# Kernel optimization log

Hardware: AMD Instinct MI355X
Metric: run time of the kernel (lower is better)

## Reference

```python
import jax, jax.numpy as jnp
import numpy as np

N, D, P, NS = 2048, 64, 32, 512  # nnodes, stop_embedding_size, preference_dim, n_active_stops
LEAKY_SLOPE = 0.01
COS_EPS = 1e-8


def setup_inputs() -> dict:
    key = jax.random.key(0)
    ks = jax.random.split(key, 10)
    dist = jax.random.uniform(ks[0], (N, N), dtype=jnp.float32)
    stops = jax.random.randint(ks[1], (NS,), 0, N)
    emb_w = jax.random.normal(ks[2], (N, D), dtype=jnp.float32) * 0.05      # nn.Embedding weight
    lin_l_w = jax.random.normal(ks[3], (P, D), dtype=jnp.float32) * 0.05    # SAGEConv lin_l (aggregated)
    lin_l_b = jnp.zeros((P,), dtype=jnp.float32)
    lin_r_w = jax.random.normal(ks[4], (P, D), dtype=jnp.float32) * 0.05    # SAGEConv lin_r (root)
    edge_w = jax.random.normal(ks[5], (2 * P,), dtype=jnp.float32) * 0.05   # edge_summarizer weight
    edge_b = jnp.zeros((), dtype=jnp.float32)
    in_len = 2 * N + 3 + P
    comb_w = jax.random.normal(ks[6], (N, in_len), dtype=jnp.float32) * 0.02  # combiner weight
    comb_b = jnp.zeros((N,), dtype=jnp.float32)
    return {
        "dist": dist, "emb_w": emb_w,
        "lin_l_w": lin_l_w, "lin_l_b": lin_l_b, "lin_r_w": lin_r_w,
        "edge_w": edge_w, "edge_b": edge_b,
        "comb_w": comb_w, "comb_b": comb_b,
        "stops": stops, "weekday": 3, "vehicles": 5,
    }


def reference(dist, emb_w, lin_l_w, lin_l_b, lin_r_w, edge_w, edge_b,
              comb_w, comb_b, stops, weekday, vehicles):
    dt = emb_w.dtype
    # --- cosine-similarity graph build ---
    norm = jnp.maximum(jnp.linalg.norm(emb_w, axis=1, keepdims=True), COS_EPS)
    xn = emb_w / norm
    sim = xn @ xn.T                                   # [N, N]
    sim = sim * (1.0 - jnp.eye(N, dtype=dt))          # fill_diagonal_(0)
    keep = jnp.zeros((N,), dtype=bool).at[stops].set(True)
    adj = ((sim > 0.5) & keep[:, None] & keep[None, :]).astype(dt)  # [N, N]
    # --- SAGEConv (mean aggregation): lin_l(mean_j x_j) + lin_r(x_i) ---
    deg = jnp.maximum(adj.sum(axis=1, keepdims=True), 1.0)
    agg = (adj @ emb_w) / deg                         # [N, D]
    pref = agg @ lin_l_w.T + lin_l_b + emb_w @ lin_r_w.T   # [N, P]
    # --- all-pairs edge summaries: Linear([pref_i, pref_j]) + LeakyReLU ---
    # equivalent to concat-then-linear, without materializing [N^2, 2P]
    a = pref @ edge_w[:P]                             # [N]
    b = pref @ edge_w[P:]                             # [N]
    es = a[:, None] + b[None, :] + edge_b             # [N, N]
    es = jnp.where(es >= 0, es, LEAKY_SLOPE * es)
    # --- combiner + log-softmax ---
    weekday_feat = jnp.full((N, 1), weekday, dtype=dt)
    vehicle_feat = jnp.full((N, 1), vehicles, dtype=dt)
    stop_feat = keep.astype(dt)[:, None]
    combined = jnp.concatenate([pref, es, dist, weekday_feat, vehicle_feat, stop_feat], axis=1)
    out = combined @ comb_w.T + comb_b                # [N, N]
    return jax.nn.log_softmax(out, axis=1)
```

## Files before the change

### kernel.cpp

```cpp
#include <hip/hip_runtime.h>

typedef unsigned short u16;
typedef __attribute__((ext_vector_type(8))) short bf16x8;
typedef __attribute__((ext_vector_type(4))) float f32x4;

__device__ __forceinline__ u16 f2bf(float f) {
    return (u16)((__float_as_uint(f) + 0x8000u) >> 16);
}

#define N_NODES 2048
#define D_EMB 64
#define P_DIM 32
#define NS_STOPS 512
#define IN_LEN 4131
#define NKT 65

#define SWZ(row, c) ((((row) * 8) + ((c) ^ ((row) & 7))) * 8)

__device__ __forceinline__ void gload16(const u16* g, u16* l) {
    __builtin_amdgcn_global_load_lds((const __attribute__((address_space(1))) void*)g,
                                     (__attribute__((address_space(3))) void*)l, 16, 0, 0);
}

__global__ __launch_bounds__(256) void k_aggpref(const float* __restrict__ emb, const int* __restrict__ stops,
                                                 const float* __restrict__ lin_l_w, const float* __restrict__ lin_l_b,
                                                 const float* __restrict__ lin_r_w, const float* __restrict__ edge_w,
                                                 float* __restrict__ pref, float* __restrict__ av, float* __restrict__ bv,
                                                 float* __restrict__ keepf) {
    __shared__ float se[NS_STOPS][68];
    __shared__ int bm[64];
    __shared__ int kl[NS_STOPS];
    __shared__ float nrm[NS_STOPS];
    __shared__ float xiS[8][D_EMB];
    __shared__ float aggS[8][D_EMB];
    __shared__ float niS[8];
    __shared__ int degS[8];
    __shared__ int kiS[8];
    __shared__ int cnt;
    int t = threadIdx.x;
    int i0 = blockIdx.x * 8;
    if (t < 64) bm[t] = 0;
    if (t == 0) cnt = 0;
    if (t < 8) degS[t] = 0;
    ((float*)aggS)[t] = 0.f;
    ((float*)aggS)[t + 256] = 0.f;
    __syncthreads();
    {
        int s0 = stops[t], s1 = stops[t + 256];
        atomicOr(&bm[s0 >> 5], 1 << (s0 & 31));
        atomicOr(&bm[s1 >> 5], 1 << (s1 & 31));
    }
    __syncthreads();
    {
        int w = bm[t >> 2];
        int base = (t >> 2) * 32 + (t & 3) * 8;
        #pragma unroll
        for (int e = 0; e < 8; ++e)
            if ((w >> ((t & 3) * 8 + e)) & 1) { int p = atomicAdd(&cnt, 1); kl[p] = base + e; }
    }
    if (t < 8) { int i = i0 + t; kiS[t] = (bm[i >> 5] >> (i & 31)) & 1; }
    {
        int n = t >> 5, d = (t & 31) * 2;
        xiS[n][d]     = emb[(i0 + n) * D_EMB + d];
        xiS[n][d + 1] = emb[(i0 + n) * D_EMB + d + 1];
    }
    __syncthreads();
    int nk = cnt;
    for (int u = t >> 3; u < nk; u += 32) {
        int l8 = (t & 7) * 8;
        f32x4 a = *(const f32x4*)&emb[kl[u] * D_EMB + l8];
        f32x4 b = *(const f32x4*)&emb[kl[u] * D_EMB + l8 + 4];
        *(f32x4*)&se[u][l8] = a;
        *(f32x4*)&se[u][l8 + 4] = b;
    }
    if (t < 8) {
        float s = 0.f;
        #pragma unroll
        for (int d = 0; d < D_EMB; ++d) s += xiS[t][d] * xiS[t][d];
        niS[t] = fmaxf(sqrtf(s), 1e-8f);
    }
    __syncthreads();
    for (int u = t; u < nk; u += 256) {
        float s = 0.f;
        #pragma unroll
        for (int d = 0; d < 16; ++d) {
            f32x4 v = *(const f32x4*)&se[u][d * 4];
            s += v[0] * v[0] + v[1] * v[1] + v[2] * v[2] + v[3] * v[3];
        }
        nrm[u] = fmaxf(sqrtf(s), 1e-8f);
    }
    __syncthreads();
    for (int u = t; u < nk; u += 256) {
        int j = kl[u];
        float nj = nrm[u];
        f32x4 er[16];
        #pragma unroll
        for (int d = 0; d < 16; ++d) er[d] = *(const f32x4*)&se[u][d * 4];
        #pragma unroll
        for (int n = 0; n < 8; ++n) {
            if (!kiS[n] || j == i0 + n) continue;
            f32x4 dv = {0.f, 0.f, 0.f, 0.f};
            #pragma unroll
            for (int d = 0; d < 16; ++d) dv += (*(const f32x4*)&xiS[n][d * 4]) * er[d];
            float dot = dv[0] + dv[1] + dv[2] + dv[3];
            if (dot > 0.5f * niS[n] * nj) {
                atomicAdd(&degS[n], 1);
                #pragma unroll
                for (int d = 0; d < 16; ++d) {
                    atomicAdd(&aggS[n][d * 4 + 0], er[d][0]);
                    atomicAdd(&aggS[n][d * 4 + 1], er[d][1]);
                    atomicAdd(&aggS[n][d * 4 + 2], er[d][2]);
                    atomicAdd(&aggS[n][d * 4 + 3], er[d][3]);
                }
            }
        }
    }
    __syncthreads();
    {
        int n = t >> 5, p = t & 31;
        int i = i0 + n;
        float inv = kiS[n] ? (1.f / fmaxf((float)degS[n], 1.0f)) : 0.f;
        float s = lin_l_b[p];
        const float* wl = &lin_l_w[p * D_EMB];
        const float* wr = &lin_r_w[p * D_EMB];
        #pragma unroll
        for (int d = 0; d < D_EMB; ++d) s += aggS[n][d] * inv * wl[d] + xiS[n][d] * wr[d];
        pref[i * P_DIM + p] = s;
        float a = s * edge_w[p];
        float b = s * edge_w[P_DIM + p];
        #pragma unroll
        for (int off = 16; off; off >>= 1) { a += __shfl_xor(a, off, 32); b += __shfl_xor(b, off, 32); }
        if (p == 0) { av[i] = a; bv[i] = b; keepf[i] = (float)kiS[n]; }
    }
}

__global__ __launch_bounds__(256) void k_pack(const float* __restrict__ comb_w, const float* __restrict__ comb_b,
                                              const int* __restrict__ wk_p, const int* __restrict__ vh_p,
                                              const float* __restrict__ dist, const float* __restrict__ pref,
                                              const float* __restrict__ av, const float* __restrict__ bv,
                                              const float* __restrict__ edge_b,
                                              u16* __restrict__ Bp, u16* __restrict__ Ap,
                                              float* __restrict__ cvec, float* __restrict__ w3) {
    int kt = blockIdx.x;
    int ty = blockIdx.y;
    int t = threadIdx.x;
    if (ty < 16) {
        int nt = ty;
        u16* tb = Bp + ((size_t)nt * NKT + kt) * 8192;
        #pragma unroll
        for (int it = 0; it < 4; ++it) {
            int q = t + it * 256;
            int r = q >> 3, c = q & 7;
            int j = nt * 128 + r;
            int k0 = kt * 64 + c * 8;
            const float* cw = comb_w + (size_t)j * IN_LEN;
            bf16x8 v;
            if (k0 < 4096) {
                f32x4 f0, f1;
                __builtin_memcpy(&f0, cw + 32 + k0, 16);
                __builtin_memcpy(&f1, cw + 36 + k0, 16);
                #pragma unroll
                for (int e = 0; e < 4; ++e) { v[e] = (short)f2bf(f0[e]); v[4 + e] = (short)f2bf(f1[e]); }
            } else if (k0 < 4128) {
                f32x4 f0, f1;
                __builtin_memcpy(&f0, cw + (k0 - 4096), 16);
                __builtin_memcpy(&f1, cw + (k0 - 4092), 16);
                #pragma unroll
                for (int e = 0; e < 4; ++e) { v[e] = (short)f2bf(f0[e]); v[4 + e] = (short)f2bf(f1[e]); }
            } else {
                #pragma unroll
                for (int e = 0; e < 8; ++e) v[e] = 0;
            }
            *(bf16x8*)&tb[r * 64 + ((c ^ (r & 7)) * 8)] = v;
        }
        if (kt == 64 && t < 128) {
            int j = nt * 128 + t;
            const float* cw = comb_w + (size_t)j * IN_LEN;
            float wk = (float)wk_p[0], vh = (float)vh_p[0];
            cvec[j] = wk * cw[4128] + vh * cw[4129] + comb_b[j];
            w3[j] = cw[4130];
        }
    } else {
        int rt = ty - 16;
        u16* ta = Ap + ((size_t)rt * NKT + kt) * 4096;
        float eb = edge_b[0];
        #pragma unroll
        for (int it = 0; it < 2; ++it) {
            int q = t + it * 256;
            int r = q >> 3, c = q & 7;
            int row = rt * 64 + r;
            int k0 = kt * 64 + c * 8;
            bf16x8 v;
            if (k0 < 2048) {
                float ab = av[row] + eb;
                f32x4 f0 = *(const f32x4*)(bv + k0);
                f32x4 f1 = *(const f32x4*)(bv + k0 + 4);
                #pragma unroll
                for (int e = 0; e < 4; ++e) {
                    float s0 = ab + f0[e]; s0 = (s0 >= 0.f) ? s0 : 0.01f * s0;
                    float s1 = ab + f1[e]; s1 = (s1 >= 0.f) ? s1 : 0.01f * s1;
                    v[e] = (short)f2bf(s0); v[4 + e] = (short)f2bf(s1);
                }
            } else if (k0 < 4096) {
                const f32x4* dp = (const f32x4*)(dist + (size_t)row * 2048 + (k0 - 2048));
                f32x4 f0 = dp[0], f1 = dp[1];
                #pragma unroll
                for (int e = 0; e < 4; ++e) { v[e] = (short)f2bf(f0[e]); v[4 + e] = (short)f2bf(f1[e]); }
            } else if (k0 < 4128) {
                const f32x4* pp = (const f32x4*)(pref + (size_t)row * P_DIM + (k0 - 4096));
                f32x4 f0 = pp[0], f1 = pp[1];
                #pragma unroll
                for (int e = 0; e < 4; ++e) { v[e] = (short)f2bf(f0[e]); v[4 + e] = (short)f2bf(f1[e]); }
            } else {
                #pragma unroll
                for (int e = 0; e < 8; ++e) v[e] = 0;
            }
            *(bf16x8*)&ta[r * 64 + ((c ^ (r & 7)) * 8)] = v;
        }
    }
}

__global__ __launch_bounds__(256, 4) void k_gemm_d(const u16* __restrict__ Ap, const u16* __restrict__ Bp,
                                                   const float* __restrict__ cvec, const float* __restrict__ w3,
                                                   const float* __restrict__ keepf,
                                                   float* __restrict__ Cout) {
    __shared__ __attribute__((aligned(16))) short As[2][4096];
    __shared__ __attribute__((aligned(16))) short Bs[2][4096];
    int t = threadIdx.x;
    int b = blockIdx.x;
    int c = b & 7, u = b >> 3;
    int mt = (c & 1) * 16 + (u & 15);
    int nt = (c >> 1) * 8 + (u >> 4);
    int tileM = mt * 64, tileN = nt * 64;
    int lane = t & 63;
    int wid = t >> 6;
    int waveM = wid & 1, waveN = wid >> 1;
    int l16 = lane & 15, quad = lane >> 4;

    f32x4 acc[2][2];
    #pragma unroll
    for (int a_ = 0; a_ < 2; ++a_)
        #pragma unroll
        for (int b_ = 0; b_ < 2; ++b_) acc[a_][b_] = (f32x4){0.f, 0.f, 0.f, 0.f};

    const u16* gA = Ap + ((size_t)mt * NKT) * 4096 + t * 8;
    const u16* gB = Bp + ((size_t)(nt >> 1) * NKT) * 8192 + (nt & 1) * 4096 + t * 8;

#define ISSUE(ktv, bb) do { \
        const u16* a0 = gA + (size_t)(ktv) * 4096; \
        const u16* b0 = gB + (size_t)(ktv) * 8192; \
        u16* ad = (u16*)As[bb] + t * 8; \
        u16* bd = (u16*)Bs[bb] + t * 8; \
        gload16(a0, ad); \
        gload16(a0 + 2048, ad + 2048); \
        gload16(b0, bd); \
        gload16(b0 + 2048, bd + 2048); \
    } while (0)

    ISSUE(0, 0);

    int cur = 0;
    for (int kt = 0; kt < NKT; ++kt) {
        __syncthreads();
        if (kt + 1 < NKT) ISSUE(kt + 1, cur ^ 1);
        const short* Asc = As[cur];
        const short* Bsc = Bs[cur];
        #pragma unroll
        for (int kk = 0; kk < 64; kk += 32) {
            int cbase = kk >> 3;
            bf16x8 af[2], bfr[2];
            #pragma unroll
            for (int mi = 0; mi < 2; ++mi) {
                int row = waveM * 32 + mi * 16 + l16;
                af[mi] = *(const bf16x8*)&Asc[SWZ(row, cbase + quad)];
            }
            #pragma unroll
            for (int ni = 0; ni < 2; ++ni) {
                int row = waveN * 32 + ni * 16 + l16;
                bfr[ni] = *(const bf16x8*)&Bsc[SWZ(row, cbase + quad)];
            }
            #pragma unroll
            for (int mi = 0; mi < 2; ++mi)
                #pragma unroll
                for (int ni = 0; ni < 2; ++ni)
                    acc[mi][ni] = __builtin_amdgcn_mfma_f32_16x16x32_bf16(af[mi], bfr[ni], acc[mi][ni], 0, 0, 0);
        }
        cur ^= 1;
    }
#undef ISSUE
    #pragma unroll
    for (int mi = 0; mi < 2; ++mi)
        #pragma unroll
        for (int ni = 0; ni < 2; ++ni) {
            int row0 = tileM + waveM * 32 + mi * 16 + quad * 4;
            int col = tileN + waveN * 32 + ni * 16 + l16;
            float cv = cvec[col], wv = w3[col];
            float* cp = Cout + (size_t)row0 * N_NODES + col;
            #pragma unroll
            for (int rr = 0; rr < 4; ++rr)
                cp[(size_t)rr * N_NODES] = acc[mi][ni][rr] + cv + keepf[row0 + rr] * wv;
        }
}

__global__ __launch_bounds__(256) void k_epi(float* __restrict__ out) {
    int i = blockIdx.x, t = threadIdx.x;
    __shared__ float redmax[4], redsum[4];
    f32x4* orow = (f32x4*)(out + (size_t)i * N_NODES);
    f32x4 v0 = orow[t];
    f32x4 v1 = orow[t + 256];
    float vmax = fmaxf(fmaxf(fmaxf(v0[0], v0[1]), fmaxf(v0[2], v0[3])),
                       fmaxf(fmaxf(v1[0], v1[1]), fmaxf(v1[2], v1[3])));
    #pragma unroll
    for (int off = 32; off; off >>= 1) vmax = fmaxf(vmax, __shfl_xor(vmax, off, 64));
    if ((t & 63) == 0) redmax[t >> 6] = vmax;
    __syncthreads();
    vmax = fmaxf(fmaxf(redmax[0], redmax[1]), fmaxf(redmax[2], redmax[3]));
    float se = 0.f;
    #pragma unroll
    for (int e = 0; e < 4; ++e) se += expf(v0[e] - vmax) + expf(v1[e] - vmax);
    #pragma unroll
    for (int off = 32; off; off >>= 1) se += __shfl_xor(se, off, 64);
    if ((t & 63) == 0) redsum[t >> 6] = se;
    __syncthreads();
    se = redsum[0] + redsum[1] + redsum[2] + redsum[3];
    float lz = vmax + logf(se);
    orow[t] = v0 - lz;
    orow[t + 256] = v1 - lz;
}

extern "C" void kernel_launch(void* const* d_in, const int* in_sizes, int n_in,
                              void* d_out, int out_size, void* d_ws, size_t ws_size,
                              hipStream_t stream) {
    const float* dist    = (const float*)d_in[0];
    const float* emb     = (const float*)d_in[1];
    const float* lin_l_w = (const float*)d_in[2];
    const float* lin_l_b = (const float*)d_in[3];
    const float* lin_r_w = (const float*)d_in[4];
    const float* edge_w  = (const float*)d_in[5];
    const float* edge_b  = (const float*)d_in[6];
    const float* comb_w  = (const float*)d_in[7];
    const float* comb_b  = (const float*)d_in[8];
    const int* stops     = (const int*)d_in[9];
    const int* wk        = (const int*)d_in[10];
    const int* vh        = (const int*)d_in[11];

    char* ws = (char*)d_ws;
    float* pref  = (float*)(ws + 0);
    float* av    = (float*)(ws + 262144);
    float* bv    = (float*)(ws + 270336);
    float* cvec  = (float*)(ws + 278528);
    float* w3    = (float*)(ws + 286720);
    float* keepf = (float*)(ws + 294912);
    u16*   Ap    = (u16*)(ws + 303104);
    u16*   Bp    = (u16*)(ws + 17342464);
    float* out   = (float*)d_out;

    hipLaunchKernelGGL(k_aggpref, dim3(256),    dim3(256), 0, stream, emb, stops,
                       lin_l_w, lin_l_b, lin_r_w, edge_w, pref, av, bv, keepf);
    hipLaunchKernelGGL(k_pack,    dim3(65, 48), dim3(256), 0, stream, comb_w, comb_b, wk, vh,
                       dist, pref, av, bv, edge_b, Bp, Ap, cvec, w3);
    hipLaunchKernelGGL(k_gemm_d,  dim3(1024),   dim3(256), 0, stream, Ap, Bp, cvec, w3, keepf, out);
    hipLaunchKernelGGL(k_epi,     dim3(2048),   dim3(256), 0, stream, out);
}
```

Measured before the change: 188.8 us.

## Load A operand fragments directly from global into registers in MFMA order

```diff
diff --git a/kernel.cpp b/kernel.cpp
--- a/kernel.cpp
+++ b/kernel.cpp
@@ -187,9 +187,9 @@
         #pragma unroll
         for (int it = 0; it < 2; ++it) {
             int q = t + it * 256;
-            int r = q >> 3, c = q & 7;
+            int r = q >> 3, kc = q & 7;
             int row = rt * 64 + r;
-            int k0 = kt * 64 + c * 8;
+            int k0 = kt * 64 + kc * 8;
             bf16x8 v;
             if (k0 < 2048) {
                 float ab = av[row] + eb;
@@ -215,7 +215,8 @@
                 #pragma unroll
                 for (int e = 0; e < 8; ++e) v[e] = 0;
             }
-            *(bf16x8*)&ta[r * 64 + ((c ^ (r & 7)) * 8)] = v;
+            int dst = ((((r >> 4) * 2 + (kc >> 2)) * 64) + (kc & 3) * 16 + (r & 15)) * 8;
+            *(bf16x8*)&ta[dst] = v;
         }
     }
 }
@@ -224,7 +225,6 @@
                                                    const float* __restrict__ cvec, const float* __restrict__ w3,
                                                    const float* __restrict__ keepf,
                                                    float* __restrict__ Cout) {
-    __shared__ __attribute__((aligned(16))) short As[2][4096];
     __shared__ __attribute__((aligned(16))) short Bs[2][4096];
     int t = threadIdx.x;
     int b = blockIdx.x;
@@ -243,37 +243,43 @@
         #pragma unroll
         for (int b_ = 0; b_ < 2; ++b_) acc[a_][b_] = (f32x4){0.f, 0.f, 0.f, 0.f};
 
-    const u16* gA = Ap + ((size_t)mt * NKT) * 4096 + t * 8;
+    const u16* gA = Ap + ((size_t)mt * NKT) * 4096 + lane * 8;
     const u16* gB = Bp + ((size_t)(nt >> 1) * NKT) * 8192 + (nt & 1) * 4096 + t * 8;
 
-#define ISSUE(ktv, bb) do { \
-        const u16* a0 = gA + (size_t)(ktv) * 4096; \
+#define ISSUEB(ktv, bb) do { \
         const u16* b0 = gB + (size_t)(ktv) * 8192; \
-        u16* ad = (u16*)As[bb] + t * 8; \
         u16* bd = (u16*)Bs[bb] + t * 8; \
-        gload16(a0, ad); \
-        gload16(a0 + 2048, ad + 2048); \
         gload16(b0, bd); \
         gload16(b0 + 2048, bd + 2048); \
     } while (0)
 
-    ISSUE(0, 0);
+    ISSUEB(0, 0);
+    bf16x8 a_cur[2][2];
+    #pragma unroll
+    for (int mi = 0; mi < 2; ++mi)
+        #pragma unroll
+        for (int cb = 0; cb < 2; ++cb)
+            a_cur[mi][cb] = *(const bf16x8*)&gA[((waveM * 2 + mi) * 2 + cb) * 512];
 
     int cur = 0;
     for (int kt = 0; kt < NKT; ++kt) {
+        bf16x8 a_nxt[2][2];
         __syncthreads();
-        if (kt + 1 < NKT) ISSUE(kt + 1, cur ^ 1);
-        const short* Asc = As[cur];
+        if (kt + 1 < NKT) {
+            ISSUEB(kt + 1, cur ^ 1);
+            const u16* gAn = gA + (size_t)(kt + 1) * 4096;
+            #pragma unroll
+            for (int mi = 0; mi < 2; ++mi)
+                #pragma unroll
+                for (int cb = 0; cb < 2; ++cb)
+                    a_nxt[mi][cb] = *(const bf16x8*)&gAn[((waveM * 2 + mi) * 2 + cb) * 512];
+        }
         const short* Bsc = Bs[cur];
         #pragma unroll
         for (int kk = 0; kk < 64; kk += 32) {
             int cbase = kk >> 3;
-            bf16x8 af[2], bfr[2];
-            #pragma unroll
-            for (int mi = 0; mi < 2; ++mi) {
-                int row = waveM * 32 + mi * 16 + l16;
-                af[mi] = *(const bf16x8*)&Asc[SWZ(row, cbase + quad)];
-            }
+            int cb = kk >> 5;
+            bf16x8 bfr[2];
             #pragma unroll
             for (int ni = 0; ni < 2; ++ni) {
                 int row = waveN * 32 + ni * 16 + l16;
@@ -283,11 +289,17 @@
             for (int mi = 0; mi < 2; ++mi)
                 #pragma unroll
                 for (int ni = 0; ni < 2; ++ni)
-                    acc[mi][ni] = __builtin_amdgcn_mfma_f32_16x16x32_bf16(af[mi], bfr[ni], acc[mi][ni], 0, 0, 0);
-        }
+                    acc[mi][ni] = __builtin_amdgcn_mfma_f32_16x16x32_bf16(
+                        cb ? a_cur[mi][1] : a_cur[mi][0], bfr[ni], acc[mi][ni], 0, 0, 0);
+        }
+        #pragma unroll
+        for (int mi = 0; mi < 2; ++mi)
+            #pragma unroll
+            for (int cb = 0; cb < 2; ++cb)
+                a_cur[mi][cb] = a_nxt[mi][cb];
         cur ^= 1;
     }
-#undef ISSUE
+#undef ISSUEB
     #pragma unroll
     for (int mi = 0; mi < 2; ++mi)
         #pragma unroll
```

New measurement: 198.7 us. 5.2% more time.
